# Optimization experiments

Hardware: AMD Instinct MI355X
Metric: run time of the kernel (lower is better)

The kernel has to match this reference:

```python
import jax, jax.numpy as jnp
import numpy as np

K_CORR = 2048        # num_correspondences (init kwarg)
MAX_CORR = 8192      # static pad size for the variable-length nonzero output
THRES_START = 0.5
THRES_STEP = 0.01


def setup_inputs() -> dict:
    key = jax.random.key(0)
    k1, k2, k3 = jax.random.split(key, 3)
    N = M = 8193  # 8192 superpoints + 1 dustbin
    # shift so exp(scores) is mostly well below the 0.5 starting threshold,
    # making the iterative threshold search actually iterate (as in practice
    # with log-domain OT scores)
    matching_scores = jax.random.normal(k1, (N, M), dtype=jnp.float32) - 5.0
    ref_n2p_scores_c = jax.random.uniform(k2, (N - 1,), dtype=jnp.float32)
    src_n2p_scores_c = jax.random.uniform(k3, (M - 1,), dtype=jnp.float32)
    return {
        "matching_scores": matching_scores,
        "ref_n2p_scores_c": ref_n2p_scores_c,
        "src_n2p_scores_c": src_n2p_scores_c,
    }


def _find_thres(inner, k):
    """Replicates: while count(score[:-1,:-1] > thres) < k: thres -= 0.01."""
    def cond(t):
        return jnp.sum(inner > t) < k
    def body(t):
        return t - jnp.float32(THRES_STEP)
    return jax.lax.while_loop(cond, body, jnp.float32(THRES_START))


def reference(matching_scores, ref_n2p_scores_c, src_n2p_scores_c):
    s = jnp.exp(matching_scores)
    # n2p reweighting of the non-dustbin block, as in the torch in-place update
    inner = s[:-1, :-1] * (ref_n2p_scores_c[:, None] * src_n2p_scores_c[None, :])
    # threshold search is discrete -> not differentiated
    thres = _find_thres(jax.lax.stop_gradient(inner), K_CORR)
    mask = inner > thres
    count = jnp.sum(mask)
    # torch returns variable-length nonzero in row-major order; we pad to MAX_CORR
    r, c = jnp.nonzero(mask, size=MAX_CORR, fill_value=0)
    valid = jnp.arange(MAX_CORR) < count
    corr_scores = jnp.where(valid, inner[r, c], 0.0)
    ref_corr_indices = jnp.where(valid, r, -1)
    src_corr_indices = jnp.where(valid, c, -1)
    return ref_corr_indices, src_corr_indices, corr_scores
```

## Files before the change

### kernel.cpp

```cpp
#include <hip/hip_runtime.h>

#define NROWS 8192
#define NCOLS 8192
#define LD    8193
#define NBINS 64
#define KCORR 2048
#define MAXC  8192
#define CAP   192
#define RPB   4
#define FCUT_LOG (-2.5257286443082556f)

__device__ __forceinline__ float inner_val(float m, float rr, float sc) {
    float p = rr * sc;
    return expf(m) * p;
}

__global__ void init_kernel(float* __restrict__ out, unsigned* __restrict__ hist,
                            unsigned* __restrict__ ovfl) {
    int i = blockIdx.x * blockDim.x + threadIdx.x;
    if (i < 2 * MAXC)       out[i] = -1.0f;
    else if (i < 3 * MAXC)  out[i] = 0.0f;
    if (i < NBINS) hist[i] = 0u;
    if (i == NBINS) *ovfl = 0u;
}

__global__ __launch_bounds__(256) void hist_kernel(
    const float* __restrict__ ms, const float* __restrict__ refs,
    const float* __restrict__ srcs, unsigned* __restrict__ hist,
    unsigned* __restrict__ candcnt, unsigned* __restrict__ cand_col,
    float* __restrict__ cand_v, unsigned* __restrict__ ovfl, int use_cand)
{
    __shared__ float t[NBINS];
    __shared__ unsigned sub[NBINS];
    __shared__ unsigned cnt[RPB];
    __shared__ uint2 pairs[RPB * CAP];
    int tid = threadIdx.x;
    if (tid == 0) {
        float tv = 0.5f;
        for (int n = 0; n < NBINS; ++n) { t[n] = tv; tv = tv - 0.01f; }
    }
    if (tid < NBINS) sub[tid] = 0u;
    if (tid < RPB) cnt[tid] = 0u;
    __syncthreads();

    int r0 = blockIdx.x * RPB;

    auto push = [&](int r, int col, float m) {
        unsigned slot = atomicAdd(&cnt[r], 1u);
        if (slot < CAP)
            pairs[r * CAP + slot] = make_uint2((unsigned)col, __float_as_uint(m));
    };

#define ISSUE(b, R0, R1, R2, R3) do {                                          \
        constexpr int r_ = (b) >> 1, h_ = (b) & 1;                             \
        int row_ = r0 + r_;                                                    \
        int s_ = (4 - (row_ & 3)) & 3;              \
        const float4* p4_ = (const float4*)(ms + (size_t)row_ * LD + s_);      \
        int i0_ = h_ * 1024 + tid;                                             \
        R0 = p4_[i0_];                                                         \
        R1 = p4_[i0_ + 256];                                                   \
        R2 = p4_[i0_ + 512];                                                   \
        if (h_ == 1) {                                                         \
            int nb_ = (NCOLS - s_) >> 2;              \
            if (i0_ + 768 < nb_) R3 = p4_[i0_ + 768];                          \
            else R3 = make_float4(-1e30f, -1e30f, -1e30f, -1e30f);             \
        } else {                                                               \
            R3 = p4_[i0_ + 768];                                               \
        }                                                                      \
    } while (0)

#define PROC(r_, c0_, q_) do {                                                 \
        bool a0 = (q_).x > FCUT_LOG, a1 = (q_).y > FCUT_LOG;                   \
        bool a2 = (q_).z > FCUT_LOG, a3 = (q_).w > FCUT_LOG;                   \
        if (a0 | a1 | a2 | a3) {                    \
            if (a0) push(r_, (c0_) + 0, (q_).x);                               \
            if (a1) push(r_, (c0_) + 1, (q_).y);                               \
            if (a2) push(r_, (c0_) + 2, (q_).z);                               \
            if (a3) push(r_, (c0_) + 3, (q_).w);                               \
        }                                                                      \
    } while (0)

#define CONSUME(b, R0, R1, R2, R3) do {                                        \
        constexpr int r_ = (b) >> 1, h_ = (b) & 1;                             \
        int s_ = (4 - ((r0 + r_) & 3)) & 3;                                    \
        int cb_ = s_ + 4 * (h_ * 1024 + tid);                                  \
        PROC(r_, cb_ + 0,    R0);                                              \
        PROC(r_, cb_ + 1024, R1);                                              \
        PROC(r_, cb_ + 2048, R2);                                              \
        PROC(r_, cb_ + 3072, R3);                                              \
    } while (0)

    float4 A0, A1, A2, A3, B0, B1, B2, B3, C0, C1, C2, C3;
    ISSUE(0, A0, A1, A2, A3);
    ISSUE(1, B0, B1, B2, B3);
    ISSUE(2, C0, C1, C2, C3);
    CONSUME(0, A0, A1, A2, A3);
    ISSUE(3, A0, A1, A2, A3);
    CONSUME(1, B0, B1, B2, B3);
    ISSUE(4, B0, B1, B2, B3);
    CONSUME(2, C0, C1, C2, C3);
    ISSUE(5, C0, C1, C2, C3);
    CONSUME(3, A0, A1, A2, A3);
    ISSUE(6, A0, A1, A2, A3);
    CONSUME(4, B0, B1, B2, B3);
    ISSUE(7, B0, B1, B2, B3);
    CONSUME(5, C0, C1, C2, C3);
    CONSUME(6, A0, A1, A2, A3);
    CONSUME(7, B0, B1, B2, B3);

#undef ISSUE
#undef PROC
#undef CONSUME

    if (tid < RPB * 8) {
        int r = tid >> 3, e = tid & 7;
        int row = r0 + r;
        int s = (4 - (row & 3)) & 3;
        int nb = (NCOLS - s) >> 2;
        int done = s + 4 * nb;
        int col = -1;
        if (e < s) col = e;
        else if (e - s < NCOLS - done) col = done + (e - s);
        if (col >= 0) {
            float m = ms[(size_t)row * LD + col];
            if (m > FCUT_LOG) push(r, col, m);
        }
    }
    __syncthreads();

    for (int r = 0; r < RPB; ++r) {
        int row = r0 + r;
        unsigned C = cnt[r];
        unsigned Cc = (C < CAP) ? C : CAP;
        float rr = refs[row];
        for (unsigned i = tid; i < Cc; i += 256) {
            uint2 pr = pairs[r * CAP + i];
            int col = (int)pr.x;
            float m = __uint_as_float(pr.y);
            float v = inner_val(m, rr, srcs[col]);
            int g = (int)floorf((0.5f - v) * 100.0f) + 1;
            g = (g < 0) ? 0 : ((g > NBINS) ? NBINS : g);
            while (g < NBINS && t[g] >= v) ++g;
            while (g > 0 && t[g - 1] < v) --g;
            atomicAdd(&sub[g], 1u);
            if (use_cand) {
                cand_col[(size_t)row * CAP + i] = (unsigned)col;
                cand_v[(size_t)row * CAP + i]   = v;
            }
        }
        if (tid == 0) {
            if (use_cand) candcnt[row] = C;
            if (C > CAP) atomicOr(ovfl, 1u);
        }
    }
    __syncthreads();

    if (tid < 64) {
        unsigned v = sub[tid];
        unsigned p = v;
        #pragma unroll
        for (int off = 1; off < 64; off <<= 1) {
            unsigned u = __shfl_up(p, off);
            if (tid >= off) p += u;
        }
        unsigned binned = __shfl(p, 63);
        unsigned g = (tid == 63) ? (v + (unsigned)(RPB * NCOLS) - binned) : v;
        if (g) atomicAdd(&hist[tid], g);
    }
}

__global__ void mid_kernel(const unsigned* __restrict__ hist,
                           float* __restrict__ thres, unsigned* __restrict__ nstar) {
    int tid = threadIdx.x;
    if (tid < 64) {
        unsigned h = hist[tid];
        unsigned cum = h;
        #pragma unroll
        for (int off = 1; off < 64; off <<= 1) {
            unsigned u = __shfl_up(cum, off);
            if (tid >= off) cum += u;
        }
        unsigned long long mk = __ballot(cum >= (unsigned)KCORR);
        int nsel = mk ? (int)(__ffsll((unsigned long long)mk) - 1) : (NBINS - 1);
        if (tid == 0) {
            float tv = 0.5f;
            for (int n = 0; n < nsel; ++n) tv = tv - 0.01f;
            *thres = tv;
            *nstar = (unsigned)nsel;
        }
    }
}

__global__ __launch_bounds__(256) void count_kernel(
    const float* __restrict__ ms, const float* __restrict__ refs,
    const float* __restrict__ srcs, const float* __restrict__ thresp,
    const unsigned* __restrict__ nstar, const unsigned* __restrict__ ovfl,
    const unsigned* __restrict__ candcnt, const float* __restrict__ cand_v,
    unsigned* __restrict__ rowcnt, int use_cand)
{
    __shared__ unsigned tot;
    int ns = (int)*nstar;
    bool fast = (use_cand && ns <= 41 && *ovfl == 0u);
    float th = *thresp;

    if (fast) {
        int tid = threadIdx.x, wv = tid >> 6, lane = tid & 63;
        int row = blockIdx.x * 4 + wv;
        unsigned C = candcnt[row];
        unsigned c = 0;
        if (C <= CAP) {
            const float* cv = cand_v + (size_t)row * CAP;
            for (unsigned i = lane; i < C; i += 64)
                c += (cv[i] > th) ? 1u : 0u;
        } else {
            float rr = refs[row];
            const float* mrow = ms + (size_t)row * LD;
            for (int col = lane; col < NCOLS; col += 64)
                c += (inner_val(mrow[col], rr, srcs[col]) > th) ? 1u : 0u;
        }
        #pragma unroll
        for (int off = 32; off > 0; off >>= 1) c += __shfl_down(c, off);
        if (lane == 0) rowcnt[row] = c;
        return;
    }

    for (int r4 = 0; r4 < 4; ++r4) {
        int row = blockIdx.x * 4 + r4;
        if (threadIdx.x == 0) tot = 0;
        __syncthreads();
        float rr = refs[row];
        const float* mrow = ms + (size_t)row * LD;
        unsigned c = 0;
        for (int col = threadIdx.x; col < NCOLS; col += 256)
            c += (inner_val(mrow[col], rr, srcs[col]) > th) ? 1u : 0u;
        atomicAdd(&tot, c);
        __syncthreads();
        if (threadIdx.x == 0) rowcnt[row] = tot;
        __syncthreads();
    }
}

__global__ __launch_bounds__(1024) void scan_kernel(
    const unsigned* __restrict__ rowcnt, unsigned* __restrict__ rowoff)
{
    __shared__ unsigned ssum[1024];
    int tid = threadIdx.x;
    int r0 = tid * 8;
    unsigned c[8], s = 0;
    #pragma unroll
    for (int k = 0; k < 8; ++k) { c[k] = rowcnt[r0 + k]; s += c[k]; }
    ssum[tid] = s;
    __syncthreads();
    for (int off = 1; off < 1024; off <<= 1) {
        unsigned v = (tid >= off) ? ssum[tid - off] : 0u;
        __syncthreads();
        ssum[tid] += v;
        __syncthreads();
    }
    unsigned excl = ssum[tid] - s;
    #pragma unroll
    for (int k = 0; k < 8; ++k) { rowoff[r0 + k] = excl; excl += c[k]; }
    if (tid == 1023) rowoff[NROWS] = excl;
}

__global__ __launch_bounds__(256) void cwrite_kernel(
    const float* __restrict__ ms, const float* __restrict__ refs,
    const float* __restrict__ srcs, const float* __restrict__ thresp,
    const unsigned* __restrict__ nstar, const unsigned* __restrict__ ovfl,
    const unsigned* __restrict__ rowoff, const unsigned* __restrict__ candcnt,
    const unsigned* __restrict__ cand_col, const float* __restrict__ cand_v,
    float* __restrict__ out, int use_cand)
{
    __shared__ unsigned s_col[4][64];
    __shared__ float    s_val[4][64];
    int tid = threadIdx.x, wv = tid >> 6, lane = tid & 63;
    int row = blockIdx.x * 4 + wv;
    unsigned base = rowoff[row], next = rowoff[row + 1];
    if (base == next || base >= MAXC) return;
    float th = *thresp;
    int ns = (int)*nstar;
    unsigned k = next - base;
    bool full = (!use_cand) || (ns >= 42) || (*ovfl != 0u) ||
                (candcnt[row] > CAP) || (k > 64);

    if (!full) {
        unsigned C = candcnt[row];
        const unsigned* cc = cand_col + (size_t)row * CAP;
        const float*    cv = cand_v  + (size_t)row * CAP;
        unsigned nrun = 0;
        for (unsigned c0 = 0; c0 < C; c0 += 64) {
            unsigned i = c0 + lane;
            bool sel = false; unsigned col = 0; float v = 0.f;
            if (i < C) { col = cc[i]; v = cv[i]; sel = (v > th); }
            unsigned long long mk = __ballot(sel);
            if (sel) {
                unsigned idx = nrun + (unsigned)__popcll(mk & ((1ull << lane) - 1ull));
                if (idx < 64) { s_col[wv][idx] = col; s_val[wv][idx] = v; }
            }
            nrun += (unsigned)__popcll(mk);
        }
        __builtin_amdgcn_s_waitcnt(0);
        __builtin_amdgcn_wave_barrier();
        unsigned kk = (nrun < k) ? nrun : k;
        if (kk > 64) kk = 64;
        if (lane < (int)kk) {
            unsigned mycol = s_col[wv][lane];
            float    myval = s_val[wv][lane];
            unsigned rank = 0;
            for (unsigned j = 0; j < kk; ++j)
                rank += (s_col[wv][j] < mycol) ? 1u : 0u;
            unsigned pos = base + rank;
            if (pos < MAXC) {
                out[pos]            = (float)row;
                out[MAXC + pos]     = (float)mycol;
                out[2 * MAXC + pos] = myval;
            }
        }
        return;
    }

    float rr = refs[row];
    const float* mrow = ms + (size_t)row * LD;
    unsigned running = base;
    for (int c0 = 0; c0 < NCOLS && running < next && running < MAXC; c0 += 64) {
        int col = c0 + lane;
        float v = inner_val(mrow[col], rr, srcs[col]);
        bool pred = v > th;
        unsigned long long mk = __ballot(pred);
        if (pred) {
            unsigned pos = running + (unsigned)__popcll(mk & ((1ull << lane) - 1ull));
            if (pos < MAXC) {
                out[pos]            = (float)row;
                out[MAXC + pos]     = (float)col;
                out[2 * MAXC + pos] = v;
            }
        }
        running += (unsigned)__popcll(mk);
    }
}

extern "C" void kernel_launch(void* const* d_in, const int* in_sizes, int n_in,
                              void* d_out, int out_size, void* d_ws, size_t ws_size,
                              hipStream_t stream) {
    const float* ms  = (const float*)d_in[0];
    const float* ref = (const float*)d_in[1];
    const float* src = (const float*)d_in[2];
    float* out = (float*)d_out;

    char* w = (char*)d_ws;
    unsigned* hist   = (unsigned*)(w);
    float*    thres  = (float*)(w + 256);
    unsigned* nstar  = (unsigned*)(w + 260);
    unsigned* ovfl   = (unsigned*)(w + 264);
    unsigned* rowcnt = (unsigned*)(w + 512);
    unsigned* rowoff = (unsigned*)(w + 512 + NROWS * 4);
    size_t cc_off = 512 + (size_t)NROWS * 4 + (size_t)(NROWS + 1) * 4;
    cc_off = (cc_off + 255) & ~(size_t)255;
    unsigned* candcnt  = (unsigned*)(w + cc_off);
    size_t col_off = cc_off + (size_t)NROWS * 4;
    unsigned* cand_col = (unsigned*)(w + col_off);
    size_t cv_off = col_off + (size_t)NROWS * CAP * 4;
    float* cand_v      = (float*)(w + cv_off);
    size_t end_off = cv_off + (size_t)NROWS * CAP * 4;

    int use_cand = (ws_size >= end_off) ? 1 : 0;

    init_kernel<<<96, 256, 0, stream>>>(out, hist, ovfl);
    hist_kernel<<<NROWS / RPB, 256, 0, stream>>>(ms, ref, src, hist, candcnt,
                                                 cand_col, cand_v, ovfl, use_cand);
    mid_kernel<<<1, 64, 0, stream>>>(hist, thres, nstar);
    count_kernel<<<NROWS / 4, 256, 0, stream>>>(ms, ref, src, thres, nstar,
                                                ovfl, candcnt, cand_v, rowcnt,
                                                use_cand);
    scan_kernel<<<1, 1024, 0, stream>>>(rowcnt, rowoff);
    cwrite_kernel<<<NROWS / 4, 256, 0, stream>>>(ms, ref, src, thres, nstar,
                                                 ovfl, rowoff, candcnt, cand_col,
                                                 cand_v, out, use_cand);
}
```

Before: 382.7 us.

## Fold threshold selection into count/write kernels and use wave-shuffle scan

Removes the single-block mid_kernel launch by having every wave in count_kernel and cwrite_kernel recompute the threshold and bin index from the 64-bin histogram using a shuffle scan. The block-wide prefix scan in scan_kernel changes from a shared-memory Hillis-Steele loop with many barriers to a wave shuffle scan plus a small cross-wave pass. hist_kernel also gets a min-blocks-per-CU launch bound. The aim is to cut one launch and the barrier latency, at the cost of redundant histogram reads and scan work in every wave.

```diff
diff --git a/kernel.cpp b/kernel.cpp
--- a/kernel.cpp
+++ b/kernel.cpp
@@ -15,6 +15,23 @@
     return expf(m) * p;
 }
 
+__device__ __forceinline__ void wave_thres(const unsigned* __restrict__ hist,
+                                           float* th_out, int* ns_out) {
+    int lane = threadIdx.x & 63;
+    unsigned cum = hist[lane];
+    #pragma unroll
+    for (int off = 1; off < 64; off <<= 1) {
+        unsigned u = __shfl_up(cum, off);
+        if (lane >= off) cum += u;
+    }
+    unsigned long long mk = __ballot(cum >= (unsigned)KCORR);
+    int nsel = mk ? (int)(__ffsll((unsigned long long)mk) - 1) : (NBINS - 1);
+    float tv = 0.5f;
+    for (int n = 0; n < nsel; ++n) tv = tv - 0.01f;
+    *th_out = tv;
+    *ns_out = nsel;
+}
+
 __global__ void init_kernel(float* __restrict__ out, unsigned* __restrict__ hist,
                             unsigned* __restrict__ ovfl) {
     int i = blockIdx.x * blockDim.x + threadIdx.x;
@@ -24,7 +41,7 @@
     if (i == NBINS) *ovfl = 0u;
 }
 
-__global__ __launch_bounds__(256) void hist_kernel(
+__global__ __launch_bounds__(256, 2) void hist_kernel(
     const float* __restrict__ ms, const float* __restrict__ refs,
     const float* __restrict__ srcs, unsigned* __restrict__ hist,
     unsigned* __restrict__ candcnt, unsigned* __restrict__ cand_col,
@@ -169,39 +186,17 @@
     }
 }
 
-__global__ void mid_kernel(const unsigned* __restrict__ hist,
-                           float* __restrict__ thres, unsigned* __restrict__ nstar) {
-    int tid = threadIdx.x;
-    if (tid < 64) {
-        unsigned h = hist[tid];
-        unsigned cum = h;
-        #pragma unroll
-        for (int off = 1; off < 64; off <<= 1) {
-            unsigned u = __shfl_up(cum, off);
-            if (tid >= off) cum += u;
-        }
-        unsigned long long mk = __ballot(cum >= (unsigned)KCORR);
-        int nsel = mk ? (int)(__ffsll((unsigned long long)mk) - 1) : (NBINS - 1);
-        if (tid == 0) {
-            float tv = 0.5f;
-            for (int n = 0; n < nsel; ++n) tv = tv - 0.01f;
-            *thres = tv;
-            *nstar = (unsigned)nsel;
-        }
-    }
-}
-
 __global__ __launch_bounds__(256) void count_kernel(
     const float* __restrict__ ms, const float* __restrict__ refs,
-    const float* __restrict__ srcs, const float* __restrict__ thresp,
-    const unsigned* __restrict__ nstar, const unsigned* __restrict__ ovfl,
-    const unsigned* __restrict__ candcnt, const float* __restrict__ cand_v,
-    unsigned* __restrict__ rowcnt, int use_cand)
+    const float* __restrict__ srcs, const unsigned* __restrict__ hist,
+    const unsigned* __restrict__ ovfl, const unsigned* __restrict__ candcnt,
+    const float* __restrict__ cand_v, unsigned* __restrict__ rowcnt,
+    int use_cand)
 {
     __shared__ unsigned tot;
-    int ns = (int)*nstar;
+    float th; int ns;
+    wave_thres(hist, &th, &ns);
     bool fast = (use_cand && ns <= 41 && *ovfl == 0u);
-    float th = *thresp;
 
     if (fast) {
         int tid = threadIdx.x, wv = tid >> 6, lane = tid & 63;
@@ -243,21 +238,31 @@
 __global__ __launch_bounds__(1024) void scan_kernel(
     const unsigned* __restrict__ rowcnt, unsigned* __restrict__ rowoff)
 {
-    __shared__ unsigned ssum[1024];
-    int tid = threadIdx.x;
+    __shared__ unsigned wsum[16];
+    int tid = threadIdx.x, lane = tid & 63, wv = tid >> 6;
     int r0 = tid * 8;
     unsigned c[8], s = 0;
     #pragma unroll
     for (int k = 0; k < 8; ++k) { c[k] = rowcnt[r0 + k]; s += c[k]; }
-    ssum[tid] = s;
-    __syncthreads();
-    for (int off = 1; off < 1024; off <<= 1) {
-        unsigned v = (tid >= off) ? ssum[tid - off] : 0u;
-        __syncthreads();
-        ssum[tid] += v;
-        __syncthreads();
-    }
-    unsigned excl = ssum[tid] - s;
+    unsigned p = s;
+    #pragma unroll
+    for (int off = 1; off < 64; off <<= 1) {
+        unsigned u = __shfl_up(p, off);
+        if (lane >= off) p += u;
+    }
+    if (lane == 63) wsum[wv] = p;
+    __syncthreads();
+    if (wv == 0 && lane < 16) {
+        unsigned w = wsum[lane];
+        #pragma unroll
+        for (int off = 1; off < 16; off <<= 1) {
+            unsigned u = __shfl_up(w, off);
+            if (lane >= off) w += u;
+        }
+        wsum[lane] = w;
+    }
+    __syncthreads();
+    unsigned excl = (wv > 0 ? wsum[wv - 1] : 0u) + (p - s);
     #pragma unroll
     for (int k = 0; k < 8; ++k) { rowoff[r0 + k] = excl; excl += c[k]; }
     if (tid == 1023) rowoff[NROWS] = excl;
@@ -265,11 +270,10 @@
 
 __global__ __launch_bounds__(256) void cwrite_kernel(
     const float* __restrict__ ms, const float* __restrict__ refs,
-    const float* __restrict__ srcs, const float* __restrict__ thresp,
-    const unsigned* __restrict__ nstar, const unsigned* __restrict__ ovfl,
-    const unsigned* __restrict__ rowoff, const unsigned* __restrict__ candcnt,
-    const unsigned* __restrict__ cand_col, const float* __restrict__ cand_v,
-    float* __restrict__ out, int use_cand)
+    const float* __restrict__ srcs, const unsigned* __restrict__ hist,
+    const unsigned* __restrict__ ovfl, const unsigned* __restrict__ rowoff,
+    const unsigned* __restrict__ candcnt, const unsigned* __restrict__ cand_col,
+    const float* __restrict__ cand_v, float* __restrict__ out, int use_cand)
 {
     __shared__ unsigned s_col[4][64];
     __shared__ float    s_val[4][64];
@@ -277,8 +281,8 @@
     int row = blockIdx.x * 4 + wv;
     unsigned base = rowoff[row], next = rowoff[row + 1];
     if (base == next || base >= MAXC) return;
-    float th = *thresp;
-    int ns = (int)*nstar;
+    float th; int ns;
+    wave_thres(hist, &th, &ns);
     unsigned k = next - base;
     bool full = (!use_cand) || (ns >= 42) || (*ovfl != 0u) ||
                 (candcnt[row] > CAP) || (k > 64);
@@ -349,8 +353,6 @@
 
     char* w = (char*)d_ws;
     unsigned* hist   = (unsigned*)(w);
-    float*    thres  = (float*)(w + 256);
-    unsigned* nstar  = (unsigned*)(w + 260);
     unsigned* ovfl   = (unsigned*)(w + 264);
     unsigned* rowcnt = (unsigned*)(w + 512);
     unsigned* rowoff = (unsigned*)(w + 512 + NROWS * 4);
@@ -368,12 +370,10 @@
     init_kernel<<<96, 256, 0, stream>>>(out, hist, ovfl);
     hist_kernel<<<NROWS / RPB, 256, 0, stream>>>(ms, ref, src, hist, candcnt,
                                                  cand_col, cand_v, ovfl, use_cand);
-    mid_kernel<<<1, 64, 0, stream>>>(hist, thres, nstar);
-    count_kernel<<<NROWS / 4, 256, 0, stream>>>(ms, ref, src, thres, nstar,
-                                                ovfl, candcnt, cand_v, rowcnt,
-                                                use_cand);
+    count_kernel<<<NROWS / 4, 256, 0, stream>>>(ms, ref, src, hist, ovfl,
+                                                candcnt, cand_v, rowcnt, use_cand);
     scan_kernel<<<1, 1024, 0, stream>>>(rowcnt, rowoff);
-    cwrite_kernel<<<NROWS / 4, 256, 0, stream>>>(ms, ref, src, thres, nstar,
-                                                 ovfl, rowoff, candcnt, cand_col,
+    cwrite_kernel<<<NROWS / 4, 256, 0, stream>>>(ms, ref, src, hist, ovfl,
+                                                 rowoff, candcnt, cand_col,
                                                  cand_v, out, use_cand);
 }
```

New measurement: 380.6 us. No clear change (-0.6%).
